# Performance work log

Hardware: AMD Instinct MI355X
Metric: run time of the kernel (lower is better)

## Reference

```python
import jax, jax.numpy as jnp
import numpy as np

N = 8192   # num_nodes
K = 64     # neighbors per node
BN_EPS = 1e-3  # keras BatchNormalization default epsilon


def setup_inputs() -> dict:
    key = jax.random.key(0)
    ks = jax.random.split(key, 8)
    input_data = jax.random.normal(ks[0], (1, N), dtype=jnp.float32)
    adj = jax.random.randint(ks[1], (N, K), 0, N, dtype=jnp.int64)
    edge_weights = jax.random.uniform(ks[2], (N, K), dtype=jnp.float32)
    # update_fn = BatchNorm -> Dropout(inference: identity) -> Dense(N, gelu) on [1, 2N]
    W = jax.random.normal(ks[3], (2 * N, N), dtype=jnp.float32) * 0.02
    b = jnp.zeros((N,), dtype=jnp.float32)
    bn_gamma = jnp.ones((2 * N,), dtype=jnp.float32)
    bn_beta = jnp.zeros((2 * N,), dtype=jnp.float32)
    bn_mean = jnp.zeros((2 * N,), dtype=jnp.float32)
    bn_var = jnp.ones((2 * N,), dtype=jnp.float32)
    return {"input_data": input_data, "adj": adj, "edge_weights": edge_weights,
            "W": W, "b": b, "bn_gamma": bn_gamma, "bn_beta": bn_beta,
            "bn_mean": bn_mean, "bn_var": bn_var}


def reference(input_data, adj, edge_weights, W, b, bn_gamma, bn_beta, bn_mean, bn_var):
    x = input_data[0]                    # [N] per-node expression
    ngh_sum = jnp.sum(x[adj], axis=1)    # gather [N,K] then sum over neighbors -> [N]
    agg = x + ngh_sum                    # 'sum' aggregation adds self
    h = jnp.concatenate([x, agg])[None, :]  # 'concat' combination -> [1, 2N]
    # BatchNorm (inference mode, moving stats)
    h = (h - bn_mean) * jax.lax.rsqrt(bn_var + BN_EPS) * bn_gamma + bn_beta
    # Dropout is identity at inference; Dense with exact (erf) gelu as in tf.nn.gelu
    out = jax.nn.gelu(h @ W + b, approximate=False)  # [1, N]
    return out
```

## Files before the change

kernel.cpp:

```cpp
#include <hip/hip_runtime.h>
#include <math.h>

#define BN_EPS 1e-3f
#define GEMV_ROWS 128
#define GEMV_COLS 1024

__global__ void agg_bn_kernel(const float* __restrict__ x,
                              const int* __restrict__ adj,
                              const float* __restrict__ bn_gamma,
                              const float* __restrict__ bn_beta,
                              const float* __restrict__ bn_mean,
                              const float* __restrict__ bn_var,
                              float* __restrict__ h_bn,
                              int N, int K)
{
    int gid  = blockIdx.x * blockDim.x + threadIdx.x;
    int node = gid >> 6;
    int lane = gid & 63;
    if (node >= N) return;

    float s = 0.0f;
    for (int k = lane; k < K; k += 64) {
        int nb = adj[(size_t)node * K + k];
        s += x[nb];
    }
#pragma unroll
    for (int off = 32; off > 0; off >>= 1)
        s += __shfl_down(s, off, 64);

    if (lane == 0) {
        float xi  = x[node];
        float agg = xi + s;
        {
            float sc = rsqrtf(bn_var[node] + BN_EPS) * bn_gamma[node];
            h_bn[node] = (xi - bn_mean[node]) * sc + bn_beta[node];
        }
        {
            int j = N + node;
            float sc = rsqrtf(bn_var[j] + BN_EPS) * bn_gamma[j];
            h_bn[j] = (agg - bn_mean[j]) * sc + bn_beta[j];
        }
    }
}

__global__ void gemv_partial_kernel(const float* __restrict__ h,
                                    const float* __restrict__ W,
                                    float* __restrict__ acc,
                                    int N)
{
    __shared__ float hs[GEMV_ROWS];
    int row0 = blockIdx.y * GEMV_ROWS;
    for (int i = threadIdx.x; i < GEMV_ROWS; i += blockDim.x)
        hs[i] = h[row0 + i];
    __syncthreads();

    int col = blockIdx.x * GEMV_COLS + threadIdx.x * 4;
    const float* Wp = W + (size_t)row0 * N + col;

    float ax = 0.0f, ay = 0.0f, az = 0.0f, aw = 0.0f;
#pragma unroll 4
    for (int r = 0; r < GEMV_ROWS; ++r) {
        float4 w = *(const float4*)(Wp + (size_t)r * N);
        float hv = hs[r];
        ax = fmaf(hv, w.x, ax);
        ay = fmaf(hv, w.y, ay);
        az = fmaf(hv, w.z, az);
        aw = fmaf(hv, w.w, aw);
    }
    atomicAdd(&acc[col + 0], ax);
    atomicAdd(&acc[col + 1], ay);
    atomicAdd(&acc[col + 2], az);
    atomicAdd(&acc[col + 3], aw);
}

__global__ void bias_gelu_kernel(const float* __restrict__ acc,
                                 const float* __restrict__ b,
                                 float* __restrict__ out, int N)
{
    int j = blockIdx.x * blockDim.x + threadIdx.x;
    if (j < N) {
        float v = acc[j] + b[j];
        out[j] = 0.5f * v * (1.0f + erff(v * 0.70710678118654752f));
    }
}

extern "C" void kernel_launch(void* const* d_in, const int* in_sizes, int n_in,
                              void* d_out, int out_size, void* d_ws, size_t ws_size,
                              hipStream_t stream)
{
    const float* x   = (const float*)d_in[0];
    const int*   adj = (const int*)d_in[1];
    const float* W   = (const float*)d_in[3];
    const float* b   = (const float*)d_in[4];
    const float* g   = (const float*)d_in[5];
    const float* be  = (const float*)d_in[6];
    const float* mn  = (const float*)d_in[7];
    const float* vr  = (const float*)d_in[8];
    float* out = (float*)d_out;

    int N = in_sizes[0];
    int K = in_sizes[1] / N;

    float* acc  = (float*)d_ws;
    float* h_bn = acc + N;

    hipMemsetAsync(acc, 0, (size_t)N * sizeof(float), stream);

    {
        long long total_threads = (long long)N * 64;
        int threads = 256;
        int blocks = (int)((total_threads + threads - 1) / threads);
        agg_bn_kernel<<<blocks, threads, 0, stream>>>(x, adj, g, be, mn, vr, h_bn, N, K);
    }
    {
        dim3 grid(N / GEMV_COLS, (2 * N) / GEMV_ROWS);
        gemv_partial_kernel<<<grid, 256, 0, stream>>>(h_bn, W, acc, N);
    }
    bias_gelu_kernel<<<(N + 255) / 256, 256, 0, stream>>>(acc, b, out, N);
}
```

Measured before the change: 704.9 us.

## Replace GEMV atomics with partial buffer and fused reduce-bias-gelu, nontemporal W loads

The GEMV no longer atomically accumulates into a zeroed buffer. Each row-block writes its partial sums to a workspace slab, and a new kernel reduces the slabs and applies bias plus GELU, which also removes the memset. Row blocks shrink to 64, which doubles the grid, and W is streamed with nontemporal loads under launch bounds. This trades roughly 256 partial rows of extra workspace traffic for the removed atomic contention.

```diff
diff --git a/kernel.cpp b/kernel.cpp
--- a/kernel.cpp
+++ b/kernel.cpp
@@ -2,8 +2,11 @@
 #include <math.h>
 
 #define BN_EPS 1e-3f
-#define GEMV_ROWS 128
-#define GEMV_COLS 1024
+
+#define GB_ROWS 64
+#define GB_COLS 1024
+
+typedef float floatx4 __attribute__((ext_vector_type(4)));
 
 __global__ void agg_bn_kernel(const float* __restrict__ x,
                               const int* __restrict__ adj,
@@ -43,44 +46,57 @@
     }
 }
 
-__global__ void gemv_partial_kernel(const float* __restrict__ h,
-                                    const float* __restrict__ W,
-                                    float* __restrict__ acc,
-                                    int N)
+__global__ __launch_bounds__(256, 8)
+void gemv_partial_kernel(const float* __restrict__ h,
+                         const float* __restrict__ W,
+                         float* __restrict__ part,
+                         int N)
 {
-    __shared__ float hs[GEMV_ROWS];
-    int row0 = blockIdx.y * GEMV_ROWS;
-    for (int i = threadIdx.x; i < GEMV_ROWS; i += blockDim.x)
-        hs[i] = h[row0 + i];
+    __shared__ float hs[GB_ROWS];
+    int row0 = blockIdx.y * GB_ROWS;
+    if (threadIdx.x < GB_ROWS)
+        hs[threadIdx.x] = h[row0 + threadIdx.x];
     __syncthreads();
 
-    int col = blockIdx.x * GEMV_COLS + threadIdx.x * 4;
+    int col = blockIdx.x * GB_COLS + threadIdx.x * 4;
     const float* Wp = W + (size_t)row0 * N + col;
 
     float ax = 0.0f, ay = 0.0f, az = 0.0f, aw = 0.0f;
-#pragma unroll 4
-    for (int r = 0; r < GEMV_ROWS; ++r) {
-        float4 w = *(const float4*)(Wp + (size_t)r * N);
+#pragma unroll 8
+    for (int r = 0; r < GB_ROWS; ++r) {
+        floatx4 w = __builtin_nontemporal_load(
+            reinterpret_cast<const floatx4*>(Wp));
         float hv = hs[r];
         ax = fmaf(hv, w.x, ax);
         ay = fmaf(hv, w.y, ay);
         az = fmaf(hv, w.z, az);
         aw = fmaf(hv, w.w, aw);
+        Wp += N;
     }
-    atomicAdd(&acc[col + 0], ax);
-    atomicAdd(&acc[col + 1], ay);
-    atomicAdd(&acc[col + 2], az);
-    atomicAdd(&acc[col + 3], aw);
+    floatx4 o = { ax, ay, az, aw };
+    *reinterpret_cast<floatx4*>(part + (size_t)blockIdx.y * N + col) = o;
 }
 
-__global__ void bias_gelu_kernel(const float* __restrict__ acc,
-                                 const float* __restrict__ b,
-                                 float* __restrict__ out, int N)
+__global__ __launch_bounds__(256)
+void reduce_bias_gelu_kernel(const float* __restrict__ part,
+                             const float* __restrict__ b,
+                             float* __restrict__ out,
+                             int N, int RY)
 {
-    int j = blockIdx.x * blockDim.x + threadIdx.x;
-    if (j < N) {
-        float v = acc[j] + b[j];
-        out[j] = 0.5f * v * (1.0f + erff(v * 0.70710678118654752f));
+    __shared__ float sm[4][64];
+    int lane = threadIdx.x & 63;
+    int wv   = threadIdx.x >> 6;
+    int col  = blockIdx.x * 64 + lane;
+
+    float s = 0.0f;
+    for (int ry = wv; ry < RY; ry += 4)
+        s += part[(size_t)ry * N + col];
+    sm[wv][lane] = s;
+    __syncthreads();
+
+    if (threadIdx.x < 64) {
+        float v = sm[0][lane] + sm[1][lane] + sm[2][lane] + sm[3][lane] + b[col];
+        out[col] = 0.5f * v * (1.0f + erff(v * 0.70710678118654752f));
     }
 }
 
@@ -100,11 +116,10 @@
 
     int N = in_sizes[0];
     int K = in_sizes[1] / N;
+    int RY = (2 * N) / GB_ROWS;
 
-    float* acc  = (float*)d_ws;
-    float* h_bn = acc + N;
-
-    hipMemsetAsync(acc, 0, (size_t)N * sizeof(float), stream);
+    float* part = (float*)d_ws;
+    float* h_bn = part + (size_t)RY * N;
 
     {
         long long total_threads = (long long)N * 64;
@@ -113,8 +128,8 @@
         agg_bn_kernel<<<blocks, threads, 0, stream>>>(x, adj, g, be, mn, vr, h_bn, N, K);
     }
     {
-        dim3 grid(N / GEMV_COLS, (2 * N) / GEMV_ROWS);
-        gemv_partial_kernel<<<grid, 256, 0, stream>>>(h_bn, W, acc, N);
+        dim3 grid(N / GB_COLS, RY);
+        gemv_partial_kernel<<<grid, 256, 0, stream>>>(h_bn, W, part, N);
     }
-    bias_gelu_kernel<<<(N + 255) / 256, 256, 0, stream>>>(acc, b, out, N);
+    reduce_bias_gelu_kernel<<<N / 64, 256, 0, stream>>>(part, b, out, N, RY);
 }
```

Result: no change. 707.7 us (+0.4%).
